# Kernel tuning notes

Hardware: AMD Instinct MI355X
Metric: run time of the kernel (lower is better)

## Reference

```python
import jax, jax.numpy as jnp
import numpy as np

V = 50000  # vocab (output_size)
H = 512    # hidden_size
SOS = 2


def gru_cell(x, h, Wih, Whh, bih, bhh):
    # Standard PyTorch GRUCell math. x,h: [B,H]; Wih,Whh: [3H,H]; biases: [3H]
    gx = x @ Wih.T + bih
    gh = h @ Whh.T + bhh
    gx_r, gx_z, gx_n = jnp.split(gx, 3, axis=-1)
    gh_r, gh_z, gh_n = jnp.split(gh, 3, axis=-1)
    r = jax.nn.sigmoid(gx_r + gh_r)
    z = jax.nn.sigmoid(gx_z + gh_z)
    n = jnp.tanh(gx_n + r * gh_n)
    return (1.0 - z) * n + z * h


def setup_inputs() -> dict:
    key = jax.random.key(0)
    ks = jax.random.split(key, 16)
    s = 1.0 / np.sqrt(H)
    u = lambda k, shp: jax.random.uniform(k, shp, jnp.float32, -s, s)
    return {
        "cw_idxs": jax.random.randint(ks[0], (32, 256), 0, V, jnp.int32),
        "qw_idxs": jax.random.randint(ks[1], (32, 32), 0, V, jnp.int32),
        "emb_enc": jax.random.normal(ks[2], (V, H), jnp.float32) * 0.02,
        "emb_dec": jax.random.normal(ks[3], (V, H), jnp.float32) * 0.02,
        "Wih_e": u(ks[4], (3 * H, H)), "Whh_e": u(ks[5], (3 * H, H)),
        "bih_e": u(ks[6], (3 * H,)), "bhh_e": u(ks[7], (3 * H,)),
        "Wih_d": u(ks[8], (3 * H, H)), "Whh_d": u(ks[9], (3 * H, H)),
        "bih_d": u(ks[10], (3 * H,)), "bhh_d": u(ks[11], (3 * H,)),
        "Wg": u(ks[12], (H, V)), "bg": u(ks[13], (V,)),
    }


def reference(cw_idxs, qw_idxs, emb_enc, emb_dec, Wih_e, Whh_e, bih_e, bhh_e,
              Wih_d, Whh_d, bih_d, bhh_d, Wg, bg):
    B, Tenc = cw_idxs.shape
    Tdec = qw_idxs.shape[1]

    # ---- Encoder: sequential GRU over context tokens ----
    enc_x = emb_enc[cw_idxs].transpose(1, 0, 2)  # [Tenc, B, H]
    h0 = jnp.zeros((B, H), jnp.float32)

    def enc_step(h, x_t):
        h = gru_cell(x_t, h, Wih_e, Whh_e, bih_e, bhh_e)
        return h, None

    h_enc, _ = jax.lax.scan(enc_step, h0, enc_x)

    # ---- Decoder with teacher forcing: input is SOS then shifted targets ----
    dec_in = jnp.concatenate(
        [jnp.full((B, 1), SOS, jnp.int32), qw_idxs[:, :-1]], axis=1)  # [B, Tdec]
    dec_x = jax.nn.relu(emb_dec[dec_in]).transpose(1, 0, 2)  # [Tdec, B, H]
    tgt = qw_idxs.T  # [Tdec, B]

    def dec_step(carry, inp):
        h, loss = carry
        x_t, y_t = inp
        h = gru_cell(x_t, h, Wih_d, Whh_d, bih_d, bhh_d)
        logp = jax.nn.log_softmax(h @ Wg + bg, axis=-1)  # [B, V]
        step_loss = -jnp.sum(jnp.take_along_axis(logp, y_t[:, None], axis=1))
        return (h, loss + step_loss), None

    (_, total_loss), _ = jax.lax.scan(
        dec_step, (h_enc, jnp.float32(0.0)), (dec_x, tgt))
    return total_loss / Tdec
```

## Files before the change

kernel.cpp:

```cpp
#include <hip/hip_runtime.h>
#include <math.h>

#define HH   512
#define BB   32
#define TENC 256
#define TDEC 32
#define VV   50000
#define SOSTOK 2
#define G3H  1536
#define NCG  49

__device__ __forceinline__ float sigmoidf_(float x) { return 1.0f / (1.0f + expf(-x)); }

__global__ __launch_bounds__(256) void transpose_w(
    const float* __restrict__ in, float* __restrict__ out)
{
    __shared__ float tile[32][33];
    const int kt = blockIdx.x * 32;
    const int jt = blockIdx.y * 32;
    const int tx = threadIdx.x & 31, ty = threadIdx.x >> 5;
#pragma unroll
    for (int l = 0; l < 4; l++) {
        int j = jt + ty + l * 8;
        tile[ty + l * 8][tx] = in[(size_t)j * HH + kt + tx];
    }
    __syncthreads();
#pragma unroll
    for (int l = 0; l < 4; l++) {
        int k = kt + ty + l * 8;
        out[(size_t)k * G3H + jt + tx] = tile[tx][ty + l * 8];
    }
}

__global__ __launch_bounds__(256) void transpose_w4(
    const float4* __restrict__ in, float4* __restrict__ out)
{
    __shared__ float4 tile[16][17];
    const int kt = blockIdx.x * 16;
    const int jt = blockIdx.y * 16;
    const int tx = threadIdx.x & 15, ty = threadIdx.x >> 4;
    tile[ty][tx] = in[(size_t)(jt + ty) * 128 + kt + tx];
    __syncthreads();
    out[(size_t)(kt + ty) * G3H + jt + tx] = tile[tx][ty];
}

__global__ __launch_bounds__(256) void gxT_kernel(
    const int* __restrict__ idxs, const float* __restrict__ emb,
    const float* __restrict__ WT, const float* __restrict__ bias,
    float* __restrict__ out, int dec_mode)
{
    __shared__ __align__(16) float As[16][HH];
    const int tid = threadIdx.x;
    const int m0 = blockIdx.x * 16;

    for (int l = tid; l < 16 * HH; l += 256) {
        int r = l >> 9, k = l & (HH - 1);
        int m = m0 + r;
        int t = m >> 5, b = m & 31;
        int idx;
        if (dec_mode) idx = (t == 0) ? SOSTOK : idxs[b * TDEC + (t - 1)];
        else          idx = idxs[b * TENC + t];
        float v = emb[(size_t)idx * HH + k];
        if (dec_mode) v = fmaxf(v, 0.0f);
        As[r][k] = v;
    }
    __syncthreads();

    const int j0 = blockIdx.y * 1024 + tid * 4;
    if (j0 >= G3H) return;

    float acc[16][4];
#pragma unroll
    for (int r = 0; r < 16; r++)
#pragma unroll
        for (int jj = 0; jj < 4; jj++) acc[r][jj] = 0.0f;

    for (int kc = 0; kc < HH; kc += 4) {
        float4 w0 = *(const float4*)(WT + (size_t)(kc + 0) * G3H + j0);
        float4 w1 = *(const float4*)(WT + (size_t)(kc + 1) * G3H + j0);
        float4 w2 = *(const float4*)(WT + (size_t)(kc + 2) * G3H + j0);
        float4 w3 = *(const float4*)(WT + (size_t)(kc + 3) * G3H + j0);
#pragma unroll
        for (int r = 0; r < 16; r++) {
            float4 a = *(const float4*)(&As[r][kc]);
            acc[r][0] += a.x * w0.x + a.y * w1.x + a.z * w2.x + a.w * w3.x;
            acc[r][1] += a.x * w0.y + a.y * w1.y + a.z * w2.y + a.w * w3.y;
            acc[r][2] += a.x * w0.z + a.y * w1.z + a.z * w2.z + a.w * w3.z;
            acc[r][3] += a.x * w0.w + a.y * w1.w + a.z * w2.w + a.w * w3.w;
        }
    }

    float4 bv = *(const float4*)(bias + j0);
#pragma unroll
    for (int r = 0; r < 16; r++) {
        float4 o;
        o.x = acc[r][0] + bv.x;
        o.y = acc[r][1] + bv.y;
        o.z = acc[r][2] + bv.z;
        o.w = acc[r][3] + bv.w;
        *(float4*)(out + (size_t)(m0 + r) * G3H + j0) = o;
    }
}

__global__ __launch_bounds__(256) void gru_step3(
    const float4* __restrict__ WT4,
    const float* __restrict__ bhh,
    const float* __restrict__ gx_t,
    const float* __restrict__ h_in,
    float* __restrict__ h_out)
{
    __shared__ float4 hs[512];
    const int tid = threadIdx.x;
    const int bid = blockIdx.x;
    const int bq = bid & 7;
    const int it = bid >> 3;
    const int bl = tid >> 6;
    const int lane = tid & 63;
    const int kq = lane >> 4;
    const int il = lane & 15;
    const int b = bq * 4 + bl;
    const int i = it * 16 + il;

    const float4* hin4 = (const float4*)h_in;
    hs[tid]       = hin4[bq * 512 + tid];
    hs[tid + 256] = hin4[bq * 512 + tid + 256];
    __syncthreads();

    const int k4base = kq * 32;
    const float4* hb = &hs[bl * 128 + k4base];
    const float4* wr = WT4 + (size_t)k4base * G3H + i;
    const float4* wz = wr + HH;
    const float4* wn = wr + 2 * HH;

    float ar = 0.f, az = 0.f, an = 0.f;
#pragma unroll 8
    for (int m = 0; m < 32; m++) {
        float4 h4 = hb[m];
        float4 w0 = wr[(size_t)m * G3H];
        float4 w1 = wz[(size_t)m * G3H];
        float4 w2 = wn[(size_t)m * G3H];
        ar += h4.x * w0.x + h4.y * w0.y + h4.z * w0.z + h4.w * w0.w;
        az += h4.x * w1.x + h4.y * w1.y + h4.z * w1.z + h4.w * w1.w;
        an += h4.x * w2.x + h4.y * w2.y + h4.z * w2.z + h4.w * w2.w;
    }

    ar += __shfl_xor(ar, 16); az += __shfl_xor(az, 16); an += __shfl_xor(an, 16);
    ar += __shfl_xor(ar, 32); az += __shfl_xor(az, 32); an += __shfl_xor(an, 32);

    if (kq == 0) {
        float r = sigmoidf_(gx_t[b * G3H + i]            + ar + bhh[i]);
        float z = sigmoidf_(gx_t[b * G3H + HH + i]       + az + bhh[HH + i]);
        float n = tanhf    (gx_t[b * G3H + 2 * HH + i]   + r * (an + bhh[2 * HH + i]));
        float hp = h_in[b * HH + i];
        h_out[b * HH + i] = (1.0f - z) * n + z * hp;
    }
}

__global__ __launch_bounds__(256) void logits_kernel(
    const float* __restrict__ Hall,
    const float* __restrict__ Wg,
    const float* __restrict__ bg,
    const int* __restrict__ qw,
    float* __restrict__ pmax,
    float* __restrict__ psum,
    float* __restrict__ tgt_logit)
{
    __shared__ __align__(16) float As[16][HH];
    __shared__ float wred[16][4];
    const int tid = threadIdx.x;
    const int m0 = blockIdx.x * 16;
    const int lane = tid & 63, wid = tid >> 6;

    for (int l = tid; l < 16 * HH; l += 256) {
        int r = l >> 9, k = l & (HH - 1);
        As[r][k] = Hall[(size_t)(m0 + r) * HH + k];
    }
    __syncthreads();

    const int j0 = blockIdx.y * 1024 + tid * 4;
    const bool valid = (j0 < VV);

    float acc[16][4];
#pragma unroll
    for (int r = 0; r < 16; r++)
#pragma unroll
        for (int jj = 0; jj < 4; jj++) acc[r][jj] = 0.0f;

    if (valid) {
        for (int kc = 0; kc < HH; kc += 4) {
            float4 w0 = *(const float4*)(Wg + (size_t)(kc + 0) * VV + j0);
            float4 w1 = *(const float4*)(Wg + (size_t)(kc + 1) * VV + j0);
            float4 w2 = *(const float4*)(Wg + (size_t)(kc + 2) * VV + j0);
            float4 w3 = *(const float4*)(Wg + (size_t)(kc + 3) * VV + j0);
#pragma unroll
            for (int r = 0; r < 16; r++) {
                float4 a = *(const float4*)(&As[r][kc]);
                acc[r][0] += a.x * w0.x + a.y * w1.x + a.z * w2.x + a.w * w3.x;
                acc[r][1] += a.x * w0.y + a.y * w1.y + a.z * w2.y + a.w * w3.y;
                acc[r][2] += a.x * w0.z + a.y * w1.z + a.z * w2.z + a.w * w3.z;
                acc[r][3] += a.x * w0.w + a.y * w1.w + a.z * w2.w + a.w * w3.w;
            }
        }
        float4 bv = *(const float4*)(bg + j0);
#pragma unroll
        for (int r = 0; r < 16; r++) {
            acc[r][0] += bv.x; acc[r][1] += bv.y; acc[r][2] += bv.z; acc[r][3] += bv.w;
        }
#pragma unroll
        for (int r = 0; r < 16; r++) {
            int m = m0 + r, t = m >> 5, b = m & 31;
            int tj = qw[b * TDEC + t];
            if (tj >= j0 && tj < j0 + 4) tgt_logit[m] = acc[r][tj - j0];
        }
    }

    float rowmax[16];
#pragma unroll
    for (int r = 0; r < 16; r++) {
        float v = valid ? fmaxf(fmaxf(acc[r][0], acc[r][1]), fmaxf(acc[r][2], acc[r][3]))
                        : -INFINITY;
        for (int off = 32; off > 0; off >>= 1) v = fmaxf(v, __shfl_xor(v, off));
        if (lane == 0) wred[r][wid] = v;
    }
    __syncthreads();
#pragma unroll
    for (int r = 0; r < 16; r++)
        rowmax[r] = fmaxf(fmaxf(wred[r][0], wred[r][1]), fmaxf(wred[r][2], wred[r][3]));
    __syncthreads();

#pragma unroll
    for (int r = 0; r < 16; r++) {
        float s = 0.0f;
        if (valid) {
            s = expf(acc[r][0] - rowmax[r]) + expf(acc[r][1] - rowmax[r])
              + expf(acc[r][2] - rowmax[r]) + expf(acc[r][3] - rowmax[r]);
        }
        for (int off = 32; off > 0; off >>= 1) s += __shfl_xor(s, off);
        if (lane == 0) wred[r][wid] = s;
    }
    __syncthreads();

    if (tid < 16) {
        int r = tid;
        float S = wred[r][0] + wred[r][1] + wred[r][2] + wred[r][3];
        pmax[blockIdx.y * 1024 + m0 + r] = rowmax[r];
        psum[blockIdx.y * 1024 + m0 + r] = S;
    }
}

__global__ __launch_bounds__(256) void loss_kernel(
    const float* __restrict__ pmax, const float* __restrict__ psum,
    const float* __restrict__ tgt_logit, float* __restrict__ out)
{
    const int tid = threadIdx.x;
    float local = 0.0f;
    for (int m = tid; m < 1024; m += 256) {
        float M = -INFINITY;
        for (int cg = 0; cg < NCG; cg++) M = fmaxf(M, pmax[cg * 1024 + m]);
        float S = 0.0f;
        for (int cg = 0; cg < NCG; cg++) S += psum[cg * 1024 + m] * expf(pmax[cg * 1024 + m] - M);
        local += M + logf(S) - tgt_logit[m];
    }
    __shared__ float red[256];
    red[tid] = local;
    __syncthreads();
    for (int s = 128; s > 0; s >>= 1) {
        if (tid < s) red[tid] += red[tid + s];
        __syncthreads();
    }
    if (tid == 0) out[0] = red[0] / (float)TDEC;
}

extern "C" void kernel_launch(void* const* d_in, const int* in_sizes, int n_in,
                              void* d_out, int out_size, void* d_ws, size_t ws_size,
                              hipStream_t stream)
{
    const int*   cw     = (const int*)  d_in[0];
    const int*   qw     = (const int*)  d_in[1];
    const float* emb_e  = (const float*)d_in[2];
    const float* emb_d  = (const float*)d_in[3];
    const float* Wih_e  = (const float*)d_in[4];
    const float* Whh_e  = (const float*)d_in[5];
    const float* bih_e  = (const float*)d_in[6];
    const float* bhh_e  = (const float*)d_in[7];
    const float* Wih_d  = (const float*)d_in[8];
    const float* Whh_d  = (const float*)d_in[9];
    const float* bih_d  = (const float*)d_in[10];
    const float* bhh_d  = (const float*)d_in[11];
    const float* Wg     = (const float*)d_in[12];
    const float* bg     = (const float*)d_in[13];

    float* ws      = (float*)d_ws;
    float* gx_enc  = ws;
    float* gx_dec  = gx_enc + (size_t)8192 * G3H;
    float* hbuf0   = gx_dec + (size_t)1024 * G3H;
    float* hbuf1   = hbuf0 + BB * HH;
    float* h_all   = hbuf1 + BB * HH;
    float* pmax    = h_all + (size_t)1024 * HH;
    float* psum    = pmax + NCG * 1024;
    float* tgt_l   = psum + NCG * 1024;
    float* WihT_e  = tgt_l + 1024;
    float* WihT_d  = WihT_e + (size_t)HH * G3H;
    float* WhhT4_e = WihT_d + (size_t)HH * G3H;
    float* WhhT4_d = WhhT4_e + (size_t)HH * G3H;

    hipMemsetAsync(hbuf0, 0, BB * HH * sizeof(float), stream);

    transpose_w <<<dim3(16, 48), 256, 0, stream>>>(Wih_e, WihT_e);
    transpose_w <<<dim3(16, 48), 256, 0, stream>>>(Wih_d, WihT_d);
    transpose_w4<<<dim3(8, 96),  256, 0, stream>>>((const float4*)Whh_e, (float4*)WhhT4_e);
    transpose_w4<<<dim3(8, 96),  256, 0, stream>>>((const float4*)Whh_d, (float4*)WhhT4_d);

    gxT_kernel<<<dim3(512, 2), 256, 0, stream>>>(cw, emb_e, WihT_e, bih_e, gx_enc, 0);

    for (int t = 0; t < TENC; t++) {
        const float* hin = (t & 1) ? hbuf1 : hbuf0;
        float*       hout = (t & 1) ? hbuf0 : hbuf1;
        gru_step3<<<256, 256, 0, stream>>>(
            (const float4*)WhhT4_e, bhh_e, gx_enc + (size_t)t * BB * G3H, hin, hout);
    }

    gxT_kernel<<<dim3(64, 2), 256, 0, stream>>>(qw, emb_d, WihT_d, bih_d, gx_dec, 1);

    for (int t = 0; t < TDEC; t++) {
        const float* hin = (t == 0) ? hbuf0 : h_all + (size_t)(t - 1) * BB * HH;
        gru_step3<<<256, 256, 0, stream>>>(
            (const float4*)WhhT4_d, bhh_d, gx_dec + (size_t)t * BB * G3H, hin,
            h_all + (size_t)t * BB * HH);
    }

    logits_kernel<<<dim3(64, NCG), 256, 0, stream>>>(h_all, Wg, bg, qw, pmax, psum, tgt_l);

    loss_kernel<<<1, 256, 0, stream>>>(pmax, psum, tgt_l, (float*)d_out);
}
```

Before: 4.165 ms.

## Replace per-step GRU launches with persistent scan kernel using grid barrier

The 256+32 per-timestep GRU kernel launches are replaced by one persistent kernel per sequence. Each of its 256 blocks keeps its slice of Whh in LDS and synchronises with the other blocks through an atomic-counter grid barrier between timesteps. This removes per-step launch overhead and the repeated global reads of the recurrent weights. It relies on all 256 blocks being co-resident, otherwise the barrier deadlocks, and it also adds occupancy hints to the gxT and logits kernels.

```diff
diff --git a/kernel.cpp b/kernel.cpp
--- a/kernel.cpp
+++ b/kernel.cpp
@@ -9,6 +9,8 @@
 #define SOSTOK 2
 #define G3H  1536
 #define NCG  49
+#define NB   256
+#define NKQ  8
 
 __device__ __forceinline__ float sigmoidf_(float x) { return 1.0f / (1.0f + expf(-x)); }
 
@@ -44,7 +46,7 @@
     out[(size_t)(kt + ty) * G3H + jt + tx] = tile[tx][ty];
 }
 
-__global__ __launch_bounds__(256) void gxT_kernel(
+__global__ __launch_bounds__(256, 3) void gxT_kernel(
     const int* __restrict__ idxs, const float* __restrict__ emb,
     const float* __restrict__ WT, const float* __restrict__ bias,
     float* __restrict__ out, int dec_mode)
@@ -102,61 +104,117 @@
     }
 }
 
-__global__ __launch_bounds__(256) void gru_step3(
+__global__ __launch_bounds__(512, 1) void gru_scan(
     const float4* __restrict__ WT4,
     const float* __restrict__ bhh,
-    const float* __restrict__ gx_t,
-    const float* __restrict__ h_in,
-    float* __restrict__ h_out)
-{
-    __shared__ float4 hs[512];
+    const float* __restrict__ gx_all,
+    float* __restrict__ hbufA,
+    float* __restrict__ hbufB,
+    float* __restrict__ h_all,
+    int T, int mode,
+    unsigned* __restrict__ barcnt)
+{
+    __shared__ __align__(16) float4 Wlds[3 * 128 * 16];
+    __shared__ __align__(16) float4 hs[4 * 129];
+    __shared__ float part[3][NKQ][64];
+
     const int tid = threadIdx.x;
     const int bid = blockIdx.x;
     const int bq = bid & 7;
     const int it = bid >> 3;
-    const int bl = tid >> 6;
+    const int kq = tid >> 6;
     const int lane = tid & 63;
-    const int kq = lane >> 4;
+    const int bl = lane >> 4;
     const int il = lane & 15;
-    const int b = bq * 4 + bl;
-    const int i = it * 16 + il;
-
-    const float4* hin4 = (const float4*)h_in;
-    hs[tid]       = hin4[bq * 512 + tid];
-    hs[tid + 256] = hin4[bq * 512 + tid + 256];
-    __syncthreads();
-
-    const int k4base = kq * 32;
-    const float4* hb = &hs[bl * 128 + k4base];
-    const float4* wr = WT4 + (size_t)k4base * G3H + i;
-    const float4* wz = wr + HH;
-    const float4* wn = wr + 2 * HH;
-
-    float ar = 0.f, az = 0.f, an = 0.f;
-#pragma unroll 8
-    for (int m = 0; m < 32; m++) {
-        float4 h4 = hb[m];
-        float4 w0 = wr[(size_t)m * G3H];
-        float4 w1 = wz[(size_t)m * G3H];
-        float4 w2 = wn[(size_t)m * G3H];
-        ar += h4.x * w0.x + h4.y * w0.y + h4.z * w0.z + h4.w * w0.w;
-        az += h4.x * w1.x + h4.y * w1.y + h4.z * w1.z + h4.w * w1.w;
-        an += h4.x * w2.x + h4.y * w2.y + h4.z * w2.z + h4.w * w2.w;
-    }
-
-    ar += __shfl_xor(ar, 16); az += __shfl_xor(az, 16); an += __shfl_xor(an, 16);
-    ar += __shfl_xor(ar, 32); az += __shfl_xor(az, 32); an += __shfl_xor(an, 32);
-
-    if (kq == 0) {
-        float r = sigmoidf_(gx_t[b * G3H + i]            + ar + bhh[i]);
-        float z = sigmoidf_(gx_t[b * G3H + HH + i]       + az + bhh[HH + i]);
-        float n = tanhf    (gx_t[b * G3H + 2 * HH + i]   + r * (an + bhh[2 * HH + i]));
-        float hp = h_in[b * HH + i];
-        h_out[b * HH + i] = (1.0f - z) * n + z * hp;
-    }
-}
-
-__global__ __launch_bounds__(256) void logits_kernel(
+
+    for (int idx = tid; idx < 3 * 128 * 16; idx += 512) {
+        int g = idx >> 11, k4 = (idx >> 4) & 127, jl = idx & 15;
+        Wlds[idx] = WT4[(size_t)k4 * G3H + g * HH + it * 16 + jl];
+    }
+
+    const int ob = bq * 4 + (tid >> 4);
+    const int oi = it * 16 + (tid & 15);
+    float bhr = 0.f, bhz = 0.f, bhn = 0.f;
+    if (tid < 64) { bhr = bhh[oi]; bhz = bhh[HH + oi]; bhn = bhh[2 * HH + oi]; }
+
+    for (int t = 0; t < T; ++t) {
+        const float* h_in;
+        float* h_out;
+        if (mode == 0) {
+            h_in  = (t & 1) ? hbufB : hbufA;
+            h_out = (t & 1) ? hbufA : hbufB;
+        } else {
+            h_in  = (t == 0) ? hbufA : h_all + (size_t)(t - 1) * BB * HH;
+            h_out = h_all + (size_t)t * BB * HH;
+        }
+        const float* gx_t = gx_all + (size_t)t * BB * G3H;
+
+        {
+            int b = tid >> 7, rem = tid & 127;
+            hs[b * 129 + rem] = ((const float4*)h_in)[bq * 512 + tid];
+        }
+        float gxr = 0.f, gxz = 0.f, gxn = 0.f;
+        if (tid < 64) {
+            gxr = gx_t[ob * G3H + oi];
+            gxz = gx_t[ob * G3H + HH + oi];
+            gxn = gx_t[ob * G3H + 2 * HH + oi];
+        }
+        __syncthreads();
+
+        float ar = 0.f, az = 0.f, an = 0.f;
+        const float4* hp4 = &hs[bl * 129 + kq * 16];
+        const float4* w0  = &Wlds[(0 * 128 + kq * 16) * 16 + il];
+        const float4* w1  = &Wlds[(1 * 128 + kq * 16) * 16 + il];
+        const float4* w2  = &Wlds[(2 * 128 + kq * 16) * 16 + il];
+#pragma unroll
+        for (int m = 0; m < 16; ++m) {
+            float4 h4 = hp4[m];
+            float4 a4 = w0[m * 16];
+            float4 b4 = w1[m * 16];
+            float4 c4 = w2[m * 16];
+            ar += h4.x * a4.x + h4.y * a4.y + h4.z * a4.z + h4.w * a4.w;
+            az += h4.x * b4.x + h4.y * b4.y + h4.z * b4.z + h4.w * b4.w;
+            an += h4.x * c4.x + h4.y * c4.y + h4.z * c4.z + h4.w * c4.w;
+        }
+        part[0][kq][lane] = ar;
+        part[1][kq][lane] = az;
+        part[2][kq][lane] = an;
+        __syncthreads();
+
+        if (tid < 64) {
+            float sr = 0.f, sz = 0.f, sn = 0.f;
+#pragma unroll
+            for (int q = 0; q < NKQ; ++q) {
+                sr += part[0][q][tid];
+                sz += part[1][q][tid];
+                sn += part[2][q][tid];
+            }
+            float r = sigmoidf_(gxr + sr + bhr);
+            float z = sigmoidf_(gxz + sz + bhz);
+            float n = tanhf(gxn + r * (sn + bhn));
+            float hprev = ((const float*)hs)[(tid >> 4) * 516 + oi];
+            h_out[(size_t)ob * HH + oi] = (1.0f - z) * n + z * hprev;
+        }
+
+        if (t + 1 < T) {
+            __syncthreads();
+            if (tid == 0) {
+                __threadfence();
+                __hip_atomic_fetch_add(barcnt, 1u, __ATOMIC_RELEASE,
+                                       __HIP_MEMORY_SCOPE_AGENT);
+                unsigned target = (unsigned)NB * (unsigned)(t + 1);
+                while (__hip_atomic_load(barcnt, __ATOMIC_ACQUIRE,
+                                         __HIP_MEMORY_SCOPE_AGENT) < target) {
+                    __builtin_amdgcn_s_sleep(2);
+                }
+                __threadfence();
+            }
+            __syncthreads();
+        }
+    }
+}
+
+__global__ __launch_bounds__(256, 3) void logits_kernel(
     const float* __restrict__ Hall,
     const float* __restrict__ Wg,
     const float* __restrict__ bg,
@@ -303,8 +361,10 @@
     float* WihT_d  = WihT_e + (size_t)HH * G3H;
     float* WhhT4_e = WihT_d + (size_t)HH * G3H;
     float* WhhT4_d = WhhT4_e + (size_t)HH * G3H;
+    unsigned* barc = (unsigned*)(WhhT4_d + (size_t)HH * G3H);
 
     hipMemsetAsync(hbuf0, 0, BB * HH * sizeof(float), stream);
+    hipMemsetAsync(barc, 0, 2 * sizeof(unsigned), stream);
 
     transpose_w <<<dim3(16, 48), 256, 0, stream>>>(Wih_e, WihT_e);
     transpose_w <<<dim3(16, 48), 256, 0, stream>>>(Wih_d, WihT_d);
@@ -313,21 +373,13 @@
 
     gxT_kernel<<<dim3(512, 2), 256, 0, stream>>>(cw, emb_e, WihT_e, bih_e, gx_enc, 0);
 
-    for (int t = 0; t < TENC; t++) {
-        const float* hin = (t & 1) ? hbuf1 : hbuf0;
-        float*       hout = (t & 1) ? hbuf0 : hbuf1;
-        gru_step3<<<256, 256, 0, stream>>>(
-            (const float4*)WhhT4_e, bhh_e, gx_enc + (size_t)t * BB * G3H, hin, hout);
-    }
+    gru_scan<<<NB, 512, 0, stream>>>((const float4*)WhhT4_e, bhh_e, gx_enc,
+                                     hbuf0, hbuf1, (float*)nullptr, TENC, 0, barc + 0);
 
     gxT_kernel<<<dim3(64, 2), 256, 0, stream>>>(qw, emb_d, WihT_d, bih_d, gx_dec, 1);
 
-    for (int t = 0; t < TDEC; t++) {
-        const float* hin = (t == 0) ? hbuf0 : h_all + (size_t)(t - 1) * BB * HH;
-        gru_step3<<<256, 256, 0, stream>>>(
-            (const float4*)WhhT4_d, bhh_d, gx_dec + (size_t)t * BB * G3H, hin,
-            h_all + (size_t)t * BB * HH);
-    }
+    gru_scan<<<NB, 512, 0, stream>>>((const float4*)WhhT4_d, bhh_d, gx_dec,
+                                     hbuf0, (float*)nullptr, h_all, TDEC, 1, barc + 1);
 
     logits_kernel<<<dim3(64, NCG), 256, 0, stream>>>(h_all, Wg, bg, qw, pmax, psum, tgt_l);
 
```

Measured after the change: 8.001 ms. +92.1%, slower.
